# Kernel optimization log

Hardware: AMD Instinct MI355X
Metric: run time of the kernel (lower is better)

## Reference

```python
import jax, jax.numpy as jnp
import numpy as np

B, H, S, D = 2, 8, 4096, 64
EPS = 1e-12  # torch F.normalize default eps

def _l2_normalize(x):
    n = jnp.linalg.norm(x, axis=-1, keepdims=True)
    return x / jnp.maximum(n, EPS)

def setup_inputs() -> dict:
    key = jax.random.key(0)
    kq, kk, kv, km = jax.random.split(key, 4)
    return {
        "query": jax.random.normal(kq, (B, H, S, D), dtype=jnp.float32),
        "key": jax.random.normal(kk, (B, H, S, D), dtype=jnp.float32),
        "value": jax.random.normal(kv, (B, H, S, D), dtype=jnp.float32),
        "mask": jax.random.randint(km, (B, 1, 1, S), 0, 2, dtype=jnp.int32),
    }

def reference(query, key, value, mask):
    q = _l2_normalize(query)
    k = _l2_normalize(key)
    # [B,H,S,S] cosine-similarity scores
    scores = jnp.einsum("bhqd,bhkd->bhqk", q, k)
    scores = jnp.where(mask == 0, jnp.float32(-1.0), scores)
    scores = (scores + 1.0) * 0.5  # map [-1,1] -> [0,1]; masked entries -> 0
    attention = scores / jnp.sum(scores, axis=-1, keepdims=True)
    return jnp.einsum("bhqk,bhkd->bhqd", attention, value)
```

## Files before the change

### kernel.cpp

```cpp
#include <hip/hip_runtime.h>


#define S 4096
#define D 64
#define BH 16
#define FSTRIDE 4352
#define NE 4225
#define NCHM 32
#define NCHO 64
#define KSTR 36
#define QSTR 72

typedef __attribute__((ext_vector_type(8))) short short8;
typedef __attribute__((ext_vector_type(4))) short short4v;
typedef __attribute__((ext_vector_type(4))) float f32x4;

__device__ __forceinline__ float rl(float v, int l) {
    return __int_as_float(__builtin_amdgcn_readlane(__float_as_int(v), l));
}
__device__ __forceinline__ float bperm(float v, int srclane) {
    return __int_as_float(
        __builtin_amdgcn_ds_bpermute(srclane << 2, __float_as_int(v)));
}
__device__ __forceinline__ unsigned bf16h(float x) {
    unsigned u = __float_as_uint(x);
    u += 0x7FFF + ((u >> 16) & 1);
    return u >> 16;
}

__global__ __launch_bounds__(256, 4) void k_moments(
    const float* __restrict__ K, const float* __restrict__ V,
    const int* __restrict__ mask, float* __restrict__ part)
{
    __shared__ unsigned short stag[8 * 64 * KSTR];
    __shared__ float sured[4 * 132];
    float* red0 = (float*)stag;
    float* red1 = red0 + 4096;

    const int bh    = blockIdx.x;
    const int chunk = blockIdx.y;
    const int tid   = threadIdx.x;
    const int lane  = tid & 63;
    const int wave  = tid >> 6;
    const int quad  = lane >> 4;
    const int l15   = lane & 15;
    const int row0  = chunk * 128 + wave * 32;

    const float* Kh = K + (size_t)bh * S * D;
    const float* Vh = V + (size_t)bh * S * D;
    const int*   mb = mask + (bh >> 3) * S;

    const int r32 = lane & 31;
    const int c2  = lane >> 5;
    const int rowA = row0 + r32;
    float ss = 0.f;
    {
        const float4* kp = (const float4*)(Kh + (size_t)rowA * D + c2 * 32);
        #pragma unroll
        for (int i = 0; i < 8; ++i) {
            float4 kv = kp[i];
            ss = fmaf(kv.x, kv.x, ss);
            ss = fmaf(kv.y, kv.y, ss);
            ss = fmaf(kv.z, kv.z, ss);
            ss = fmaf(kv.w, kv.w, ss);
        }
    }
    ss += __shfl_xor(ss, 32, 64);
    const float mval = (float)mb[rowA];
    const float minv = mval / fmaxf(sqrtf(ss), 1e-12f);
    float nw = mval;
    nw += __shfl_xor(nw, 1, 64);  nw += __shfl_xor(nw, 2, 64);
    nw += __shfl_xor(nw, 4, 64);  nw += __shfl_xor(nw, 8, 64);
    nw += __shfl_xor(nw, 16, 64); nw += __shfl_xor(nw, 32, 64);

    unsigned short* Kst = stag + wave * (64 * KSTR);
    unsigned short* Vst = stag + 4 * (64 * KSTR) + wave * (64 * KSTR);
    unsigned* KstW = (unsigned*)Kst;
    unsigned* VstW = (unsigned*)Vst;

    float4 s4 = {0.f, 0.f, 0.f, 0.f}, u4 = {0.f, 0.f, 0.f, 0.f};
    unsigned kprev[4], vprev[4];
    #pragma unroll
    for (int i = 0; i < 8; ++i) {
        const int key = 8 * quad + i;
        const int row = row0 + key;
        float4 kf = *(const float4*)(Kh + (size_t)row * D + 4 * l15);
        float4 vf = *(const float4*)(Vh + (size_t)row * D + 4 * l15);
        float aj = bperm(minv, key);
        float mj = bperm(mval, key);
        float k0 = kf.x * aj, k1 = kf.y * aj, k2 = kf.z * aj, k3 = kf.w * aj;
        float v0 = vf.x * mj, v1 = vf.y * mj, v2 = vf.z * mj, v3 = vf.w * mj;
        s4.x += k0; s4.y += k1; s4.z += k2; s4.w += k3;
        u4.x += v0; u4.y += v1; u4.z += v2; u4.w += v3;
        unsigned kb0 = bf16h(k0), kb1 = bf16h(k1), kb2 = bf16h(k2), kb3 = bf16h(k3);
        unsigned vb0 = bf16h(v0), vb1 = bf16h(v1), vb2 = bf16h(v2), vb3 = bf16h(v3);
        if (i & 1) {
            const int base = 4 * quad + (i >> 1);
            KstW[(4 * l15 + 0) * 18 + base] = kprev[0] | (kb0 << 16);
            KstW[(4 * l15 + 1) * 18 + base] = kprev[1] | (kb1 << 16);
            KstW[(4 * l15 + 2) * 18 + base] = kprev[2] | (kb2 << 16);
            KstW[(4 * l15 + 3) * 18 + base] = kprev[3] | (kb3 << 16);
            VstW[(4 * l15 + 0) * 18 + base] = vprev[0] | (vb0 << 16);
            VstW[(4 * l15 + 1) * 18 + base] = vprev[1] | (vb1 << 16);
            VstW[(4 * l15 + 2) * 18 + base] = vprev[2] | (vb2 << 16);
            VstW[(4 * l15 + 3) * 18 + base] = vprev[3] | (vb3 << 16);
        } else {
            kprev[0] = kb0; kprev[1] = kb1; kprev[2] = kb2; kprev[3] = kb3;
            vprev[0] = vb0; vprev[1] = vb1; vprev[2] = vb2; vprev[3] = vb3;
        }
    }
    s4.x += __shfl_xor(s4.x, 16, 64); s4.x += __shfl_xor(s4.x, 32, 64);
    s4.y += __shfl_xor(s4.y, 16, 64); s4.y += __shfl_xor(s4.y, 32, 64);
    s4.z += __shfl_xor(s4.z, 16, 64); s4.z += __shfl_xor(s4.z, 32, 64);
    s4.w += __shfl_xor(s4.w, 16, 64); s4.w += __shfl_xor(s4.w, 32, 64);
    u4.x += __shfl_xor(u4.x, 16, 64); u4.x += __shfl_xor(u4.x, 32, 64);
    u4.y += __shfl_xor(u4.y, 16, 64); u4.y += __shfl_xor(u4.y, 32, 64);
    u4.z += __shfl_xor(u4.z, 16, 64); u4.z += __shfl_xor(u4.z, 32, 64);
    u4.w += __shfl_xor(u4.w, 16, 64); u4.w += __shfl_xor(u4.w, 32, 64);
    if (quad == 0) {
        sured[wave * 132 + 4 * l15 + 0]      = s4.x;
        sured[wave * 132 + 4 * l15 + 1]      = s4.y;
        sured[wave * 132 + 4 * l15 + 2]      = s4.z;
        sured[wave * 132 + 4 * l15 + 3]      = s4.w;
        sured[wave * 132 + 64 + 4 * l15 + 0] = u4.x;
        sured[wave * 132 + 64 + 4 * l15 + 1] = u4.y;
        sured[wave * 132 + 64 + 4 * l15 + 2] = u4.z;
        sured[wave * 132 + 64 + 4 * l15 + 3] = u4.w;
    }
    if (lane == 0) sured[wave * 132 + 128] = nw * 0.5f;
    __syncthreads();

    short8 af[4], bfr[4];
    #pragma unroll
    for (int t = 0; t < 4; ++t) {
        const unsigned short* ab = Kst + (t * 16 + l15) * KSTR + quad * 8;
        short4v a0 = *(const short4v*)ab;
        short4v a1 = *(const short4v*)(ab + 4);
        af[t] = __builtin_shufflevector(a0, a1, 0, 1, 2, 3, 4, 5, 6, 7);
        const unsigned short* bb = Vst + (t * 16 + l15) * KSTR + quad * 8;
        short4v b0 = *(const short4v*)bb;
        short4v b1 = *(const short4v*)(bb + 4);
        bfr[t] = __builtin_shufflevector(b0, b1, 0, 1, 2, 3, 4, 5, 6, 7);
    }
    f32x4 acc[4][4];
    #pragma unroll
    for (int tm = 0; tm < 4; ++tm)
        #pragma unroll
        for (int tn = 0; tn < 4; ++tn)
            acc[tm][tn] = (f32x4){0.f, 0.f, 0.f, 0.f};
    #pragma unroll
    for (int tn = 0; tn < 4; ++tn)
        #pragma unroll
        for (int tm = 0; tm < 4; ++tm)
            acc[tm][tn] = __builtin_amdgcn_mfma_f32_16x16x32_bf16(
                af[tm], bfr[tn], acc[tm][tn], 0, 0, 0);
    __syncthreads();

    if (wave < 2) {
        float* rd = wave ? red1 : red0;
        #pragma unroll
        for (int tm = 0; tm < 4; ++tm)
            #pragma unroll
            for (int tn = 0; tn < 4; ++tn)
                #pragma unroll
                for (int rr = 0; rr < 4; ++rr)
                    rd[(tm * 16 + quad * 4 + rr) * 64 + tn * 16 + l15]
                        = acc[tm][tn][rr];
    }
    __syncthreads();
    if (wave >= 2) {
        float* rd = (wave == 3) ? red1 : red0;
        #pragma unroll
        for (int tm = 0; tm < 4; ++tm)
            #pragma unroll
            for (int tn = 0; tn < 4; ++tn)
                #pragma unroll
                for (int rr = 0; rr < 4; ++rr)
                    rd[(tm * 16 + quad * 4 + rr) * 64 + tn * 16 + l15]
                        += acc[tm][tn][rr];
    }
    __syncthreads();

    float* pp = part + ((size_t)bh * NCHM + chunk) * FSTRIDE;
    for (int i = tid; i < NE; i += 256) {
        float v;
        if (i < 4096)
            v = red0[i] + red1[i];
        else {
            int e = i - 4096;
            v = sured[e] + sured[132 + e] + sured[264 + e] + sured[396 + e];
        }
        pp[i] = v;
    }
}

__global__ __launch_bounds__(256) void k_reduce(
    const float* __restrict__ part, float* __restrict__ fin,
    unsigned short* __restrict__ finTh)
{
    const int bh = blockIdx.x;
    const int e  = blockIdx.y * 256 + threadIdx.x;
    if (e >= NE) return;
    const float* p = part + (size_t)bh * NCHM * FSTRIDE + e;
    float a0 = 0.f, a1 = 0.f, a2 = 0.f, a3 = 0.f;
    #pragma unroll
    for (int c = 0; c < NCHM; c += 4) {
        a0 += p[(size_t)(c + 0) * FSTRIDE];
        a1 += p[(size_t)(c + 1) * FSTRIDE];
        a2 += p[(size_t)(c + 2) * FSTRIDE];
        a3 += p[(size_t)(c + 3) * FSTRIDE];
    }
    float v = (a0 + a1) + (a2 + a3);
    if (e < 4096)
        finTh[(size_t)bh * 4096 + (e & 63) * 64 + (e >> 6)] = (unsigned short)bf16h(v);
    else
        fin[(size_t)bh * FSTRIDE + e] = v;
}

__global__ __launch_bounds__(256) void k_out(
    const float* __restrict__ Q, const float* __restrict__ fin,
    const unsigned short* __restrict__ finTh, float* __restrict__ out)
{
    __shared__ unsigned short Qst[4 * 16 * QSTR];

    const int bh    = blockIdx.x;
    const int chunk = blockIdx.y;
    const int tid   = threadIdx.x;
    const int lane  = tid & 63;
    const int wave  = tid >> 6;
    const int quad  = lane >> 4;
    const int l15   = lane & 15;
    const int row0  = chunk * 64;

    const float* fb = fin + (size_t)bh * FSTRIDE;
    const unsigned short* fT = finTh + (size_t)bh * 4096;
    const float* Qh = Q + (size_t)bh * S * D;
    float*       Oh = out + (size_t)bh * S * D;

    const int rowA = row0 + wave * 16 + l15;
    float ss = 0.f, qs = 0.f;
    {
        const float4* qp = (const float4*)(Qh + (size_t)rowA * D + quad * 16);
        const float4* sp = (const float4*)(fb + 4096 + quad * 16);
        #pragma unroll
        for (int i = 0; i < 4; ++i) {
            float4 qv = qp[i], sv = sp[i];
            ss = fmaf(qv.x, qv.x, ss);
            ss = fmaf(qv.y, qv.y, ss);
            ss = fmaf(qv.z, qv.z, ss);
            ss = fmaf(qv.w, qv.w, ss);
            qs = fmaf(qv.x, sv.x, qs);
            qs = fmaf(qv.y, sv.y, qs);
            qs = fmaf(qv.z, sv.z, qs);
            qs = fmaf(qv.w, sv.w, qs);
        }
    }
    ss += __shfl_xor(ss, 16, 64); ss += __shfl_xor(ss, 32, 64);
    qs += __shfl_xor(qs, 16, 64); qs += __shfl_xor(qs, 32, 64);
    const float nval = fb[4224];
    const float invL = 1.f / fmaxf(sqrtf(ss), 1e-12f);
    const float rden = 1.f / fmaf(qs, invL, nval);

    unsigned short* Qw = Qst + wave * 16 * QSTR;
    #pragma unroll
    for (int r = 0; r < 16; ++r) {
        float qd = Qh[(size_t)(row0 + wave * 16 + r) * D + lane];
        Qw[r * QSTR + lane] = (unsigned short)bf16h(qd * rl(invL, r));
    }
    asm volatile("" ::: "memory");

    short8 af0 = *(const short8*)(Qw + l15 * QSTR + quad * 8);
    short8 af1 = *(const short8*)(Qw + l15 * QSTR + 32 + quad * 8);

    f32x4 acc[4];
    #pragma unroll
    for (int tn = 0; tn < 4; ++tn) acc[tn] = (f32x4){0.f, 0.f, 0.f, 0.f};
    #pragma unroll
    for (int tn = 0; tn < 4; ++tn) {
        short8 b0 = *(const short8*)(fT + (tn * 16 + l15) * 64 + quad * 8);
        short8 b1 = *(const short8*)(fT + (tn * 16 + l15) * 64 + 32 + quad * 8);
        acc[tn] = __builtin_amdgcn_mfma_f32_16x16x32_bf16(af0, b0, acc[tn], 0, 0, 0);
        acc[tn] = __builtin_amdgcn_mfma_f32_16x16x32_bf16(af1, b1, acc[tn], 0, 0, 0);
    }

    float u4[4];
    #pragma unroll
    for (int tn = 0; tn < 4; ++tn) u4[tn] = fb[4160 + tn * 16 + l15];

    #pragma unroll
    for (int rr = 0; rr < 4; ++rr) {
        const int src = quad * 4 + rr;
        float rd = bperm(rden, src);
        const size_t row = row0 + wave * 16 + src;
        #pragma unroll
        for (int tn = 0; tn < 4; ++tn)
            Oh[row * D + tn * 16 + l15] = (acc[tn][rr] + u4[tn]) * rd;
    }
}

extern "C" void kernel_launch(void* const* d_in, const int* in_sizes, int n_in,
                              void* d_out, int out_size, void* d_ws, size_t ws_size,
                              hipStream_t stream) {
    const float* Q    = (const float*)d_in[0];
    const float* K    = (const float*)d_in[1];
    const float* V    = (const float*)d_in[2];
    const int*   mask = (const int*)d_in[3];
    float* out = (float*)d_out;
    float* ws  = (float*)d_ws;

    float*          fin   = ws;
    unsigned short* finTh = (unsigned short*)(ws + (size_t)BH * FSTRIDE);
    float*          part  = (float*)((char*)finTh + (size_t)BH * 4096 * 2);

    k_moments<<<dim3(BH, NCHM), 256, 0, stream>>>(K, V, mask, part);
    k_reduce <<<dim3(BH, (NE + 255) / 256), 256, 0, stream>>>(part, fin, finTh);
    k_out    <<<dim3(BH, NCHO), 256, 0, stream>>>(Q, fin, finTh, out);
}
```

Baseline: 107.8 us.

## Fuse moments, reduce and output kernels into one cooperative kernel with grid syncs

Merges the three kernels (per-chunk K/V moment computation, cross-chunk reduction, and query-side output) into one cooperative kernel of 512 blocks separated by two grid.sync barriers. Each block handles two output row-chunks, reusing the reduced moment fragments held in registers. The aim is to remove two kernel launch gaps and their tail effects. In exchange it adds grid-wide barrier cost, tightens launch bounds for co-residency, and the reduce phase runs on 512 blocks with only part of the threads active.

```diff
diff --git a/kernel.cpp b/kernel.cpp
--- a/kernel.cpp
+++ b/kernel.cpp
@@ -1,4 +1,7 @@
 #include <hip/hip_runtime.h>
+#include <hip/hip_cooperative_groups.h>
+
+namespace cg = cooperative_groups;
 
 
 #define S 4096
@@ -7,9 +10,9 @@
 #define FSTRIDE 4352
 #define NE 4225
 #define NCHM 32
-#define NCHO 64
 #define KSTR 36
 #define QSTR 72
+#define SMEM_BYTES (8 * 64 * KSTR * 2 + 4 * 132 * 4)
 
 typedef __attribute__((ext_vector_type(8))) short short8;
 typedef __attribute__((ext_vector_type(4))) short short4v;
@@ -28,273 +31,285 @@
     return u >> 16;
 }
 
-__global__ __launch_bounds__(256, 4) void k_moments(
-    const float* __restrict__ K, const float* __restrict__ V,
-    const int* __restrict__ mask, float* __restrict__ part)
+__global__ __launch_bounds__(256, 3) void k_fused(
+    const float* __restrict__ Q, const float* __restrict__ K,
+    const float* __restrict__ V, const int* __restrict__ mask,
+    float* __restrict__ part, float* __restrict__ fin,
+    unsigned short* __restrict__ finTh, float* __restrict__ out)
 {
-    __shared__ unsigned short stag[8 * 64 * KSTR];
-    __shared__ float sured[4 * 132];
-    float* red0 = (float*)stag;
-    float* red1 = red0 + 4096;
-
-    const int bh    = blockIdx.x;
-    const int chunk = blockIdx.y;
-    const int tid   = threadIdx.x;
-    const int lane  = tid & 63;
-    const int wave  = tid >> 6;
-    const int quad  = lane >> 4;
-    const int l15   = lane & 15;
-    const int row0  = chunk * 128 + wave * 32;
-
-    const float* Kh = K + (size_t)bh * S * D;
-    const float* Vh = V + (size_t)bh * S * D;
-    const int*   mb = mask + (bh >> 3) * S;
-
-    const int r32 = lane & 31;
-    const int c2  = lane >> 5;
-    const int rowA = row0 + r32;
-    float ss = 0.f;
+    __shared__ __align__(16) unsigned char smem_raw[SMEM_BYTES];
+    cg::grid_group grid = cg::this_grid();
+
+    const int tid  = threadIdx.x;
+    const int lane = tid & 63;
+    const int wave = tid >> 6;
+    const int quad = lane >> 4;
+    const int l15  = lane & 15;
+
     {
-        const float4* kp = (const float4*)(Kh + (size_t)rowA * D + c2 * 32);
+        unsigned short* stag  = (unsigned short*)smem_raw;
+        float*          sured = (float*)(smem_raw + 8 * 64 * KSTR * 2);
+        float* red0 = (float*)smem_raw;
+        float* red1 = red0 + 4096;
+
+        const int bh    = blockIdx.x >> 5;
+        const int chunk = blockIdx.x & 31;
+        const int row0  = chunk * 128 + wave * 32;
+
+        const float* Kh = K + (size_t)bh * S * D;
+        const float* Vh = V + (size_t)bh * S * D;
+        const int*   mb = mask + (bh >> 3) * S;
+
+        const int r32  = lane & 31;
+        const int c2   = lane >> 5;
+        const int rowA = row0 + r32;
+        float ss = 0.f;
+        {
+            const float4* kp = (const float4*)(Kh + (size_t)rowA * D + c2 * 32);
+            #pragma unroll
+            for (int i = 0; i < 8; ++i) {
+                float4 kv = kp[i];
+                ss = fmaf(kv.x, kv.x, ss);
+                ss = fmaf(kv.y, kv.y, ss);
+                ss = fmaf(kv.z, kv.z, ss);
+                ss = fmaf(kv.w, kv.w, ss);
+            }
+        }
+        ss += __shfl_xor(ss, 32, 64);
+        const float mval = (float)mb[rowA];
+        const float minv = mval / fmaxf(sqrtf(ss), 1e-12f);
+        float nw = mval;
+        nw += __shfl_xor(nw, 1, 64);  nw += __shfl_xor(nw, 2, 64);
+        nw += __shfl_xor(nw, 4, 64);  nw += __shfl_xor(nw, 8, 64);
+        nw += __shfl_xor(nw, 16, 64); nw += __shfl_xor(nw, 32, 64);
+
+        unsigned short* Kst = stag + wave * (64 * KSTR);
+        unsigned short* Vst = stag + 4 * (64 * KSTR) + wave * (64 * KSTR);
+        unsigned* KstW = (unsigned*)Kst;
+        unsigned* VstW = (unsigned*)Vst;
+
+        float4 s4 = {0.f, 0.f, 0.f, 0.f}, u4 = {0.f, 0.f, 0.f, 0.f};
+        unsigned kprev[4], vprev[4];
         #pragma unroll
         for (int i = 0; i < 8; ++i) {
-            float4 kv = kp[i];
-            ss = fmaf(kv.x, kv.x, ss);
-            ss = fmaf(kv.y, kv.y, ss);
-            ss = fmaf(kv.z, kv.z, ss);
-            ss = fmaf(kv.w, kv.w, ss);
+            const int key = 8 * quad + i;
+            const int row = row0 + key;
+            float4 kf = *(const float4*)(Kh + (size_t)row * D + 4 * l15);
+            float4 vf = *(const float4*)(Vh + (size_t)row * D + 4 * l15);
+            float aj = bperm(minv, key);
+            float mj = bperm(mval, key);
+            float k0 = kf.x * aj, k1 = kf.y * aj, k2 = kf.z * aj, k3 = kf.w * aj;
+            float v0 = vf.x * mj, v1 = vf.y * mj, v2 = vf.z * mj, v3 = vf.w * mj;
+            s4.x += k0; s4.y += k1; s4.z += k2; s4.w += k3;
+            u4.x += v0; u4.y += v1; u4.z += v2; u4.w += v3;
+            unsigned kb0 = bf16h(k0), kb1 = bf16h(k1), kb2 = bf16h(k2), kb3 = bf16h(k3);
+            unsigned vb0 = bf16h(v0), vb1 = bf16h(v1), vb2 = bf16h(v2), vb3 = bf16h(v3);
+            if (i & 1) {
+                const int base = 4 * quad + (i >> 1);
+                KstW[(4 * l15 + 0) * 18 + base] = kprev[0] | (kb0 << 16);
+                KstW[(4 * l15 + 1) * 18 + base] = kprev[1] | (kb1 << 16);
+                KstW[(4 * l15 + 2) * 18 + base] = kprev[2] | (kb2 << 16);
+                KstW[(4 * l15 + 3) * 18 + base] = kprev[3] | (kb3 << 16);
+                VstW[(4 * l15 + 0) * 18 + base] = vprev[0] | (vb0 << 16);
+                VstW[(4 * l15 + 1) * 18 + base] = vprev[1] | (vb1 << 16);
+                VstW[(4 * l15 + 2) * 18 + base] = vprev[2] | (vb2 << 16);
+                VstW[(4 * l15 + 3) * 18 + base] = vprev[3] | (vb3 << 16);
+            } else {
+                kprev[0] = kb0; kprev[1] = kb1; kprev[2] = kb2; kprev[3] = kb3;
+                vprev[0] = vb0; vprev[1] = vb1; vprev[2] = vb2; vprev[3] = vb3;
+            }
+        }
+        s4.x += __shfl_xor(s4.x, 16, 64); s4.x += __shfl_xor(s4.x, 32, 64);
+        s4.y += __shfl_xor(s4.y, 16, 64); s4.y += __shfl_xor(s4.y, 32, 64);
+        s4.z += __shfl_xor(s4.z, 16, 64); s4.z += __shfl_xor(s4.z, 32, 64);
+        s4.w += __shfl_xor(s4.w, 16, 64); s4.w += __shfl_xor(s4.w, 32, 64);
+        u4.x += __shfl_xor(u4.x, 16, 64); u4.x += __shfl_xor(u4.x, 32, 64);
+        u4.y += __shfl_xor(u4.y, 16, 64); u4.y += __shfl_xor(u4.y, 32, 64);
+        u4.z += __shfl_xor(u4.z, 16, 64); u4.z += __shfl_xor(u4.z, 32, 64);
+        u4.w += __shfl_xor(u4.w, 16, 64); u4.w += __shfl_xor(u4.w, 32, 64);
+        if (quad == 0) {
+            sured[wave * 132 + 4 * l15 + 0]      = s4.x;
+            sured[wave * 132 + 4 * l15 + 1]      = s4.y;
+            sured[wave * 132 + 4 * l15 + 2]      = s4.z;
+            sured[wave * 132 + 4 * l15 + 3]      = s4.w;
+            sured[wave * 132 + 64 + 4 * l15 + 0] = u4.x;
+            sured[wave * 132 + 64 + 4 * l15 + 1] = u4.y;
+            sured[wave * 132 + 64 + 4 * l15 + 2] = u4.z;
+            sured[wave * 132 + 64 + 4 * l15 + 3] = u4.w;
+        }
+        if (lane == 0) sured[wave * 132 + 128] = nw * 0.5f;
+        __syncthreads();
+
+        short8 af[4], bfr[4];
+        #pragma unroll
+        for (int t = 0; t < 4; ++t) {
+            const unsigned short* ab = Kst + (t * 16 + l15) * KSTR + quad * 8;
+            short4v a0 = *(const short4v*)ab;
+            short4v a1 = *(const short4v*)(ab + 4);
+            af[t] = __builtin_shufflevector(a0, a1, 0, 1, 2, 3, 4, 5, 6, 7);
+            const unsigned short* bb = Vst + (t * 16 + l15) * KSTR + quad * 8;
+            short4v b0 = *(const short4v*)bb;
+            short4v b1 = *(const short4v*)(bb + 4);
+            bfr[t] = __builtin_shufflevector(b0, b1, 0, 1, 2, 3, 4, 5, 6, 7);
+        }
+        f32x4 acc[4][4];
+        #pragma unroll
+        for (int tm = 0; tm < 4; ++tm)
+            #pragma unroll
+            for (int tn = 0; tn < 4; ++tn)
+                acc[tm][tn] = (f32x4){0.f, 0.f, 0.f, 0.f};
+        #pragma unroll
+        for (int tn = 0; tn < 4; ++tn)
+            #pragma unroll
+            for (int tm = 0; tm < 4; ++tm)
+                acc[tm][tn] = __builtin_amdgcn_mfma_f32_16x16x32_bf16(
+                    af[tm], bfr[tn], acc[tm][tn], 0, 0, 0);
+        __syncthreads();
+
+        if (wave < 2) {
+            float* rd = wave ? red1 : red0;
+            #pragma unroll
+            for (int tm = 0; tm < 4; ++tm)
+                #pragma unroll
+                for (int tn = 0; tn < 4; ++tn)
+                    #pragma unroll
+                    for (int rr = 0; rr < 4; ++rr)
+                        rd[(tm * 16 + quad * 4 + rr) * 64 + tn * 16 + l15]
+                            = acc[tm][tn][rr];
+        }
+        __syncthreads();
+        if (wave >= 2) {
+            float* rd = (wave == 3) ? red1 : red0;
+            #pragma unroll
+            for (int tm = 0; tm < 4; ++tm)
+                #pragma unroll
+                for (int tn = 0; tn < 4; ++tn)
+                    #pragma unroll
+                    for (int rr = 0; rr < 4; ++rr)
+                        rd[(tm * 16 + quad * 4 + rr) * 64 + tn * 16 + l15]
+                            += acc[tm][tn][rr];
+        }
+        __syncthreads();
+
+        float* pp = part + ((size_t)bh * NCHM + chunk) * FSTRIDE;
+        for (int i = tid; i < NE; i += 256) {
+            float v;
+            if (i < 4096)
+                v = red0[i] + red1[i];
+            else {
+                int e = i - 4096;
+                v = sured[e] + sured[132 + e] + sured[264 + e] + sured[396 + e];
+            }
+            pp[i] = v;
         }
     }
-    ss += __shfl_xor(ss, 32, 64);
-    const float mval = (float)mb[rowA];
-    const float minv = mval / fmaxf(sqrtf(ss), 1e-12f);
-    float nw = mval;
-    nw += __shfl_xor(nw, 1, 64);  nw += __shfl_xor(nw, 2, 64);
-    nw += __shfl_xor(nw, 4, 64);  nw += __shfl_xor(nw, 8, 64);
-    nw += __shfl_xor(nw, 16, 64); nw += __shfl_xor(nw, 32, 64);
-
-    unsigned short* Kst = stag + wave * (64 * KSTR);
-    unsigned short* Vst = stag + 4 * (64 * KSTR) + wave * (64 * KSTR);
-    unsigned* KstW = (unsigned*)Kst;
-    unsigned* VstW = (unsigned*)Vst;
-
-    float4 s4 = {0.f, 0.f, 0.f, 0.f}, u4 = {0.f, 0.f, 0.f, 0.f};
-    unsigned kprev[4], vprev[4];
-    #pragma unroll
-    for (int i = 0; i < 8; ++i) {
-        const int key = 8 * quad + i;
-        const int row = row0 + key;
-        float4 kf = *(const float4*)(Kh + (size_t)row * D + 4 * l15);
-        float4 vf = *(const float4*)(Vh + (size_t)row * D + 4 * l15);
-        float aj = bperm(minv, key);
-        float mj = bperm(mval, key);
-        float k0 = kf.x * aj, k1 = kf.y * aj, k2 = kf.z * aj, k3 = kf.w * aj;
-        float v0 = vf.x * mj, v1 = vf.y * mj, v2 = vf.z * mj, v3 = vf.w * mj;
-        s4.x += k0; s4.y += k1; s4.z += k2; s4.w += k3;
-        u4.x += v0; u4.y += v1; u4.z += v2; u4.w += v3;
-        unsigned kb0 = bf16h(k0), kb1 = bf16h(k1), kb2 = bf16h(k2), kb3 = bf16h(k3);
-        unsigned vb0 = bf16h(v0), vb1 = bf16h(v1), vb2 = bf16h(v2), vb3 = bf16h(v3);
-        if (i & 1) {
-            const int base = 4 * quad + (i >> 1);
-            KstW[(4 * l15 + 0) * 18 + base] = kprev[0] | (kb0 << 16);
-            KstW[(4 * l15 + 1) * 18 + base] = kprev[1] | (kb1 << 16);
-            KstW[(4 * l15 + 2) * 18 + base] = kprev[2] | (kb2 << 16);
-            KstW[(4 * l15 + 3) * 18 + base] = kprev[3] | (kb3 << 16);
-            VstW[(4 * l15 + 0) * 18 + base] = vprev[0] | (vb0 << 16);
-            VstW[(4 * l15 + 1) * 18 + base] = vprev[1] | (vb1 << 16);
-            VstW[(4 * l15 + 2) * 18 + base] = vprev[2] | (vb2 << 16);
-            VstW[(4 * l15 + 3) * 18 + base] = vprev[3] | (vb3 << 16);
-        } else {
-            kprev[0] = kb0; kprev[1] = kb1; kprev[2] = kb2; kprev[3] = kb3;
-            vprev[0] = vb0; vprev[1] = vb1; vprev[2] = vb2; vprev[3] = vb3;
+
+    grid.sync();
+
+    {
+        const int gtid = blockIdx.x * 256 + tid;
+        if (gtid < BH * NE) {
+            const int bh = gtid / NE;
+            const int e  = gtid - bh * NE;
+            const float* p = part + (size_t)bh * NCHM * FSTRIDE + e;
+            float a0 = 0.f, a1 = 0.f, a2 = 0.f, a3 = 0.f;
+            #pragma unroll
+            for (int c = 0; c < NCHM; c += 4) {
+                a0 += p[(size_t)(c + 0) * FSTRIDE];
+                a1 += p[(size_t)(c + 1) * FSTRIDE];
+                a2 += p[(size_t)(c + 2) * FSTRIDE];
+                a3 += p[(size_t)(c + 3) * FSTRIDE];
+            }
+            float v = (a0 + a1) + (a2 + a3);
+            if (e < 4096)
+                finTh[(size_t)bh * 4096 + (e & 63) * 64 + (e >> 6)]
+                    = (unsigned short)bf16h(v);
+            else
+                fin[(size_t)bh * FSTRIDE + e] = v;
         }
     }
-    s4.x += __shfl_xor(s4.x, 16, 64); s4.x += __shfl_xor(s4.x, 32, 64);
-    s4.y += __shfl_xor(s4.y, 16, 64); s4.y += __shfl_xor(s4.y, 32, 64);
-    s4.z += __shfl_xor(s4.z, 16, 64); s4.z += __shfl_xor(s4.z, 32, 64);
-    s4.w += __shfl_xor(s4.w, 16, 64); s4.w += __shfl_xor(s4.w, 32, 64);
-    u4.x += __shfl_xor(u4.x, 16, 64); u4.x += __shfl_xor(u4.x, 32, 64);
-    u4.y += __shfl_xor(u4.y, 16, 64); u4.y += __shfl_xor(u4.y, 32, 64);
-    u4.z += __shfl_xor(u4.z, 16, 64); u4.z += __shfl_xor(u4.z, 32, 64);
-    u4.w += __shfl_xor(u4.w, 16, 64); u4.w += __shfl_xor(u4.w, 32, 64);
-    if (quad == 0) {
-        sured[wave * 132 + 4 * l15 + 0]      = s4.x;
-        sured[wave * 132 + 4 * l15 + 1]      = s4.y;
-        sured[wave * 132 + 4 * l15 + 2]      = s4.z;
-        sured[wave * 132 + 4 * l15 + 3]      = s4.w;
-        sured[wave * 132 + 64 + 4 * l15 + 0] = u4.x;
-        sured[wave * 132 + 64 + 4 * l15 + 1] = u4.y;
-        sured[wave * 132 + 64 + 4 * l15 + 2] = u4.z;
-        sured[wave * 132 + 64 + 4 * l15 + 3] = u4.w;
-    }
-    if (lane == 0) sured[wave * 132 + 128] = nw * 0.5f;
-    __syncthreads();
-
-    short8 af[4], bfr[4];
-    #pragma unroll
-    for (int t = 0; t < 4; ++t) {
-        const unsigned short* ab = Kst + (t * 16 + l15) * KSTR + quad * 8;
-        short4v a0 = *(const short4v*)ab;
-        short4v a1 = *(const short4v*)(ab + 4);
-        af[t] = __builtin_shufflevector(a0, a1, 0, 1, 2, 3, 4, 5, 6, 7);
-        const unsigned short* bb = Vst + (t * 16 + l15) * KSTR + quad * 8;
-        short4v b0 = *(const short4v*)bb;
-        short4v b1 = *(const short4v*)(bb + 4);
-        bfr[t] = __builtin_shufflevector(b0, b1, 0, 1, 2, 3, 4, 5, 6, 7);
-    }
-    f32x4 acc[4][4];
-    #pragma unroll
-    for (int tm = 0; tm < 4; ++tm)
-        #pragma unroll
-        for (int tn = 0; tn < 4; ++tn)
-            acc[tm][tn] = (f32x4){0.f, 0.f, 0.f, 0.f};
-    #pragma unroll
-    for (int tn = 0; tn < 4; ++tn)
-        #pragma unroll
-        for (int tm = 0; tm < 4; ++tm)
-            acc[tm][tn] = __builtin_amdgcn_mfma_f32_16x16x32_bf16(
-                af[tm], bfr[tn], acc[tm][tn], 0, 0, 0);
-    __syncthreads();
-
-    if (wave < 2) {
-        float* rd = wave ? red1 : red0;
-        #pragma unroll
-        for (int tm = 0; tm < 4; ++tm)
-            #pragma unroll
-            for (int tn = 0; tn < 4; ++tn)
+
+    grid.sync();
+
+    {
+        unsigned short* Qst = (unsigned short*)smem_raw;
+
+        const int bh = blockIdx.x >> 5;
+        const float* fb = fin + (size_t)bh * FSTRIDE;
+        const unsigned short* fT = finTh + (size_t)bh * 4096;
+        const float* Qh = Q + (size_t)bh * S * D;
+        float*       Oh = out + (size_t)bh * S * D;
+
+        const float nval = fb[4224];
+        float uo[4];
+        #pragma unroll
+        for (int tn = 0; tn < 4; ++tn) uo[tn] = fb[4160 + tn * 16 + l15];
+
+        short8 bf0[4], bf1[4];
+        #pragma unroll
+        for (int tn = 0; tn < 4; ++tn) {
+            bf0[tn] = *(const short8*)(fT + (tn * 16 + l15) * 64 + quad * 8);
+            bf1[tn] = *(const short8*)(fT + (tn * 16 + l15) * 64 + 32 + quad * 8);
+        }
+
+        #pragma unroll
+        for (int cc = 0; cc < 2; ++cc) {
+            const int row0 = ((blockIdx.x & 31) * 2 + cc) * 64;
+
+            const int rowA = row0 + wave * 16 + l15;
+            float ss = 0.f, qs = 0.f;
+            {
+                const float4* qp = (const float4*)(Qh + (size_t)rowA * D + quad * 16);
+                const float4* sp = (const float4*)(fb + 4096 + quad * 16);
                 #pragma unroll
-                for (int rr = 0; rr < 4; ++rr)
-                    rd[(tm * 16 + quad * 4 + rr) * 64 + tn * 16 + l15]
-                        = acc[tm][tn][rr];
-    }
-    __syncthreads();
-    if (wave >= 2) {
-        float* rd = (wave == 3) ? red1 : red0;
-        #pragma unroll
-        for (int tm = 0; tm < 4; ++tm)
-            #pragma unroll
-            for (int tn = 0; tn < 4; ++tn)
+                for (int i = 0; i < 4; ++i) {
+                    float4 qv = qp[i], sv = sp[i];
+                    ss = fmaf(qv.x, qv.x, ss);
+                    ss = fmaf(qv.y, qv.y, ss);
+                    ss = fmaf(qv.z, qv.z, ss);
+                    ss = fmaf(qv.w, qv.w, ss);
+                    qs = fmaf(qv.x, sv.x, qs);
+                    qs = fmaf(qv.y, sv.y, qs);
+                    qs = fmaf(qv.z, sv.z, qs);
+                    qs = fmaf(qv.w, sv.w, qs);
+                }
+            }
+            ss += __shfl_xor(ss, 16, 64); ss += __shfl_xor(ss, 32, 64);
+            qs += __shfl_xor(qs, 16, 64); qs += __shfl_xor(qs, 32, 64);
+            const float invL = 1.f / fmaxf(sqrtf(ss), 1e-12f);
+            const float rden = 1.f / fmaf(qs, invL, nval);
+
+            unsigned short* Qw = Qst + wave * 16 * QSTR;
+            #pragma unroll
+            for (int r = 0; r < 16; ++r) {
+                float qd = Qh[(size_t)(row0 + wave * 16 + r) * D + lane];
+                Qw[r * QSTR + lane] = (unsigned short)bf16h(qd * rl(invL, r));
+            }
+            asm volatile("" ::: "memory");
+
+            short8 af0 = *(const short8*)(Qw + l15 * QSTR + quad * 8);
+            short8 af1 = *(const short8*)(Qw + l15 * QSTR + 32 + quad * 8);
+
+            f32x4 acc[4];
+            #pragma unroll
+            for (int tn = 0; tn < 4; ++tn) acc[tn] = (f32x4){0.f, 0.f, 0.f, 0.f};
+            #pragma unroll
+            for (int tn = 0; tn < 4; ++tn) {
+                acc[tn] = __builtin_amdgcn_mfma_f32_16x16x32_bf16(af0, bf0[tn], acc[tn], 0, 0, 0);
+                acc[tn] = __builtin_amdgcn_mfma_f32_16x16x32_bf16(af1, bf1[tn], acc[tn], 0, 0, 0);
+            }
+
+            #pragma unroll
+            for (int rr = 0; rr < 4; ++rr) {
+                const int src = quad * 4 + rr;
+                float rd = bperm(rden, src);
+                const size_t row = row0 + wave * 16 + src;
                 #pragma unroll
-                for (int rr = 0; rr < 4; ++rr)
-                    rd[(tm * 16 + quad * 4 + rr) * 64 + tn * 16 + l15]
-                        += acc[tm][tn][rr];
-    }
-    __syncthreads();
-
-    float* pp = part + ((size_t)bh * NCHM + chunk) * FSTRIDE;
-    for (int i = tid; i < NE; i += 256) {
-        float v;
-        if (i < 4096)
-            v = red0[i] + red1[i];
-        else {
-            int e = i - 4096;
-            v = sured[e] + sured[132 + e] + sured[264 + e] + sured[396 + e];
-        }
-        pp[i] = v;
-    }
-}
-
-__global__ __launch_bounds__(256) void k_reduce(
-    const float* __restrict__ part, float* __restrict__ fin,
-    unsigned short* __restrict__ finTh)
-{
-    const int bh = blockIdx.x;
-    const int e  = blockIdx.y * 256 + threadIdx.x;
-    if (e >= NE) return;
-    const float* p = part + (size_t)bh * NCHM * FSTRIDE + e;
-    float a0 = 0.f, a1 = 0.f, a2 = 0.f, a3 = 0.f;
-    #pragma unroll
-    for (int c = 0; c < NCHM; c += 4) {
-        a0 += p[(size_t)(c + 0) * FSTRIDE];
-        a1 += p[(size_t)(c + 1) * FSTRIDE];
-        a2 += p[(size_t)(c + 2) * FSTRIDE];
-        a3 += p[(size_t)(c + 3) * FSTRIDE];
-    }
-    float v = (a0 + a1) + (a2 + a3);
-    if (e < 4096)
-        finTh[(size_t)bh * 4096 + (e & 63) * 64 + (e >> 6)] = (unsigned short)bf16h(v);
-    else
-        fin[(size_t)bh * FSTRIDE + e] = v;
-}
-
-__global__ __launch_bounds__(256) void k_out(
-    const float* __restrict__ Q, const float* __restrict__ fin,
-    const unsigned short* __restrict__ finTh, float* __restrict__ out)
-{
-    __shared__ unsigned short Qst[4 * 16 * QSTR];
-
-    const int bh    = blockIdx.x;
-    const int chunk = blockIdx.y;
-    const int tid   = threadIdx.x;
-    const int lane  = tid & 63;
-    const int wave  = tid >> 6;
-    const int quad  = lane >> 4;
-    const int l15   = lane & 15;
-    const int row0  = chunk * 64;
-
-    const float* fb = fin + (size_t)bh * FSTRIDE;
-    const unsigned short* fT = finTh + (size_t)bh * 4096;
-    const float* Qh = Q + (size_t)bh * S * D;
-    float*       Oh = out + (size_t)bh * S * D;
-
-    const int rowA = row0 + wave * 16 + l15;
-    float ss = 0.f, qs = 0.f;
-    {
-        const float4* qp = (const float4*)(Qh + (size_t)rowA * D + quad * 16);
-        const float4* sp = (const float4*)(fb + 4096 + quad * 16);
-        #pragma unroll
-        for (int i = 0; i < 4; ++i) {
-            float4 qv = qp[i], sv = sp[i];
-            ss = fmaf(qv.x, qv.x, ss);
-            ss = fmaf(qv.y, qv.y, ss);
-            ss = fmaf(qv.z, qv.z, ss);
-            ss = fmaf(qv.w, qv.w, ss);
-            qs = fmaf(qv.x, sv.x, qs);
-            qs = fmaf(qv.y, sv.y, qs);
-            qs = fmaf(qv.z, sv.z, qs);
-            qs = fmaf(qv.w, sv.w, qs);
-        }
-    }
-    ss += __shfl_xor(ss, 16, 64); ss += __shfl_xor(ss, 32, 64);
-    qs += __shfl_xor(qs, 16, 64); qs += __shfl_xor(qs, 32, 64);
-    const float nval = fb[4224];
-    const float invL = 1.f / fmaxf(sqrtf(ss), 1e-12f);
-    const float rden = 1.f / fmaf(qs, invL, nval);
-
-    unsigned short* Qw = Qst + wave * 16 * QSTR;
-    #pragma unroll
-    for (int r = 0; r < 16; ++r) {
-        float qd = Qh[(size_t)(row0 + wave * 16 + r) * D + lane];
-        Qw[r * QSTR + lane] = (unsigned short)bf16h(qd * rl(invL, r));
-    }
-    asm volatile("" ::: "memory");
-
-    short8 af0 = *(const short8*)(Qw + l15 * QSTR + quad * 8);
-    short8 af1 = *(const short8*)(Qw + l15 * QSTR + 32 + quad * 8);
-
-    f32x4 acc[4];
-    #pragma unroll
-    for (int tn = 0; tn < 4; ++tn) acc[tn] = (f32x4){0.f, 0.f, 0.f, 0.f};
-    #pragma unroll
-    for (int tn = 0; tn < 4; ++tn) {
-        short8 b0 = *(const short8*)(fT + (tn * 16 + l15) * 64 + quad * 8);
-        short8 b1 = *(const short8*)(fT + (tn * 16 + l15) * 64 + 32 + quad * 8);
-        acc[tn] = __builtin_amdgcn_mfma_f32_16x16x32_bf16(af0, b0, acc[tn], 0, 0, 0);
-        acc[tn] = __builtin_amdgcn_mfma_f32_16x16x32_bf16(af1, b1, acc[tn], 0, 0, 0);
-    }
-
-    float u4[4];
-    #pragma unroll
-    for (int tn = 0; tn < 4; ++tn) u4[tn] = fb[4160 + tn * 16 + l15];
-
-    #pragma unroll
-    for (int rr = 0; rr < 4; ++rr) {
-        const int src = quad * 4 + rr;
-        float rd = bperm(rden, src);
-        const size_t row = row0 + wave * 16 + src;
-        #pragma unroll
-        for (int tn = 0; tn < 4; ++tn)
-            Oh[row * D + tn * 16 + l15] = (acc[tn][rr] + u4[tn]) * rd;
+                for (int tn = 0; tn < 4; ++tn)
+                    Oh[row * D + tn * 16 + l15] = (acc[tn][rr] + uo[tn]) * rd;
+            }
+            asm volatile("" ::: "memory");
+        }
     }
 }
 
@@ -312,7 +327,8 @@
     unsigned short* finTh = (unsigned short*)(ws + (size_t)BH * FSTRIDE);
     float*          part  = (float*)((char*)finTh + (size_t)BH * 4096 * 2);
 
-    k_moments<<<dim3(BH, NCHM), 256, 0, stream>>>(K, V, mask, part);
-    k_reduce <<<dim3(BH, (NE + 255) / 256), 256, 0, stream>>>(part, fin, finTh);
-    k_out    <<<dim3(BH, NCHO), 256, 0, stream>>>(Q, fin, finTh, out);
-}
+    void* args[] = {(void*)&Q, (void*)&K, (void*)&V, (void*)&mask,
+                    (void*)&part, (void*)&fin, (void*)&finTh, (void*)&out};
+    hipLaunchCooperativeKernel((const void*)k_fused, dim3(BH * NCHM), dim3(256),
+                               args, 0, stream);
+}
```

Measured after the change: 221.8 us. 2.06x slower.
